# Performance work log

Measured on AMD Instinct MI355X. Metric: run time of the kernel, lower is better.

The kernel has to match this reference:

```python
import jax, jax.numpy as jnp
import numpy as np

D_MODEL = 1024
D_HIDDEN = 4096
NUM_EXPERT = 2
TOP_K = 1
W_SCALE = 0.02  # keep expert pre-exp outputs small so exp() in combine stays finite
EPS = float(np.finfo(float).eps)


def setup_inputs() -> dict:
    key = jax.random.key(0)
    ks = jax.random.split(key, 6)
    x = jax.random.normal(ks[0], (4, 4096, D_MODEL), dtype=jnp.float32)
    Wg = jax.random.normal(ks[1], (D_MODEL, NUM_EXPERT), dtype=jnp.float32) * W_SCALE
    bg = jax.random.normal(ks[2], (NUM_EXPERT,), dtype=jnp.float32) * W_SCALE
    We = jax.random.normal(ks[3], (NUM_EXPERT, D_MODEL, D_HIDDEN), dtype=jnp.float32) * W_SCALE
    be = jax.random.normal(ks[4], (NUM_EXPERT, D_HIDDEN), dtype=jnp.float32) * W_SCALE
    return {"x": x, "Wg": Wg, "bg": bg, "We": We, "be": be}


def reference(x, Wg, bg, We, be):
    B, N, C = x.shape
    xt = x.reshape(-1, C)                               # [T, C]
    # NaiveGate: linear -> top-k -> softmax over top-k logits -> dense scatter
    logits = xt @ Wg + bg                               # [T, E]
    top_v, top_i = jax.lax.top_k(logits, TOP_K)         # [T, k]
    top_g = jax.nn.softmax(top_v, axis=-1)              # [T, k] (==1.0 when k=1)
    gates = jnp.sum(jax.nn.one_hot(top_i, NUM_EXPERT, dtype=logits.dtype) * top_g[..., None], axis=1)  # [T, E]
    # expert FFNs (dense over all tokens; gate==0 tokens contribute nothing in combine,
    # matching SparseDispatcher semantics exactly)
    eo = jnp.einsum('tc,ech->eth', xt, We) + be[:, None, :]   # [E, T, H]
    # combine: sum_e gate[t,e] * exp(expert_e(x_t)); zeros -> eps; then log
    combined = jnp.einsum('te,eth->th', gates, jnp.exp(eo))   # [T, H]
    combined = jnp.where(combined == 0, EPS, combined)
    return jnp.log(combined).reshape(B, N, D_HIDDEN)
```

## Files before the change

kernel.cpp:

```cpp
#include <hip/hip_runtime.h>
#include <hip/hip_bf16.h>


#define DM 1024
#define DH 4096
#define KS 32
#define NS (DM / KS)

typedef __attribute__((ext_vector_type(4))) float f32x4;
typedef __attribute__((ext_vector_type(8))) __bf16 bf16x8;

__device__ __forceinline__ unsigned short f2bf(float f) {
    union { float f; unsigned u; } a; a.f = f;
    unsigned u = a.u;
    u += 0x7fffu + ((u >> 16) & 1u);
    return (unsigned short)(u >> 16);
}

__device__ __forceinline__ void gl16(const unsigned short* g, unsigned short* l) {
    __builtin_amdgcn_global_load_lds(
        (const __attribute__((address_space(1))) unsigned int*)(g),
        (__attribute__((address_space(3))) unsigned int*)(l), 16, 0, 0);
}

__global__ __launch_bounds__(1024) void prep(
    const float* __restrict__ x, const float* __restrict__ Wg,
    const float* __restrict__ bg, const float* __restrict__ We, int T,
    unsigned short* __restrict__ xbf, unsigned short* __restrict__ webt,
    int* __restrict__ perm, int* __restrict__ eidx, int* __restrict__ cur)
{
    int bid = blockIdx.x, tid = threadIdx.x;

    if (bid < 512) {
        __shared__ unsigned short tile[4][64][72];
        int sub = tid >> 8, t2 = tid & 255;
        int g = bid * 4 + sub;
        int e = g >> 10, rr = g & 1023, kt = rr >> 6, ht = rr & 63;
        int k0 = kt * 64, h0 = ht * 64;
        int k = t2 >> 2, hc = t2 & 3;
        const float* src = We + ((size_t)e * DM + k0 + k) * DH + h0 + hc * 16;
#pragma unroll
        for (int j = 0; j < 4; ++j) {
            f32x4 v = *(const f32x4*)(src + j * 4);
#pragma unroll
            for (int q = 0; q < 4; ++q)
                tile[sub][hc * 16 + j * 4 + q][k] = f2bf(v[q]);
        }
        __syncthreads();
        int h = t2 >> 2, kc = t2 & 3;
        unsigned short* dst = webt + ((size_t)e * DH + h0 + h) * DM + k0 + kc * 16;
        *(uint4*)(dst)     = *(const uint4*)&tile[sub][h][kc * 16];
        *(uint4*)(dst + 8) = *(const uint4*)&tile[sub][h][kc * 16 + 8];
        return;
    }

    __shared__ unsigned char eL[64];
    int gb = bid - 512;
    int lane = tid & 63, w = tid >> 6;
    float wgv[32];
#pragma unroll
    for (int j = 0; j < 8; ++j)
        *(f32x4*)&wgv[j * 4] = *(const f32x4*)(Wg + lane * 32 + j * 4);
    float bg0 = bg[0], bg1 = bg[1];
    int t0 = gb * 64 + w * 4;
#pragma unroll
    for (int tl = 0; tl < 4; ++tl) {
        int t = t0 + tl;
        const float* xr = x + (size_t)t * DM + lane * 16;
        double g0 = 0.0, g1 = 0.0;
        unsigned hw[8];
#pragma unroll
        for (int j = 0; j < 4; ++j) {
            f32x4 v = *(const f32x4*)(xr + j * 4);
#pragma unroll
            for (int q = 0; q < 4; ++q) {
                g0 += (double)v[q] * (double)wgv[2 * (j * 4 + q)];
                g1 += (double)v[q] * (double)wgv[2 * (j * 4 + q) + 1];
            }
            hw[j * 2]     = (unsigned)f2bf(v[0]) | ((unsigned)f2bf(v[1]) << 16);
            hw[j * 2 + 1] = (unsigned)f2bf(v[2]) | ((unsigned)f2bf(v[3]) << 16);
        }
        unsigned short* xw = xbf + (size_t)t * DM + lane * 16;
        uint4 u0; u0.x = hw[0]; u0.y = hw[1]; u0.z = hw[2]; u0.w = hw[3];
        uint4 u1; u1.x = hw[4]; u1.y = hw[5]; u1.z = hw[6]; u1.w = hw[7];
        *(uint4*)(xw)     = u0;
        *(uint4*)(xw + 8) = u1;
#pragma unroll
        for (int off = 32; off; off >>= 1) {
            g0 += __shfl_xor(g0, off);
            g1 += __shfl_xor(g1, off);
        }
        if (lane == 0) {
            int ee = ((g1 + (double)bg1) > (g0 + (double)bg0)) ? 1 : 0;
            eidx[t] = ee;
            eL[w * 4 + tl] = (unsigned char)ee;
        }
    }
    __syncthreads();
    if (w == 0) {
        int myE = eL[lane];
        unsigned long long m1 = __ballot(myE != 0);
        int tot1 = __popcll(m1);
        int b0 = 0, b1 = 0;
        if (lane == 0) {
            b0 = atomicAdd(cur, 64 - tot1);
            b1 = atomicAdd(cur + 1, tot1);
        }
        b0 = __shfl(b0, 0);
        b1 = __shfl(b1, 0);
        unsigned long long lm = (1ull << lane) - 1ull;
        int rank = __popcll((myE ? m1 : ~m1) & lm);
        int dstp = myE ? (T - b1 - tot1 + rank) : (b0 + rank);
        perm[dstp] = gb * 64 + lane;
    }
}

__global__ __launch_bounds__(256, 3) void moe_gemm(
    const unsigned short* __restrict__ xbf,
    const unsigned short* __restrict__ webt,
    const float* __restrict__ be,
    const int* __restrict__ perm,
    const int* __restrict__ eidx,
    float* __restrict__ out)
{
    __shared__ __align__(16) char smem[17408];
    unsigned short* As = (unsigned short*)smem;
    unsigned short* Bs = (unsigned short*)(smem + 8192);

    const int nwg = gridDim.x;
    const int bid = blockIdx.x;
    const int swz = (bid & 7) * (nwg >> 3) + (bid >> 3);
    const int mt = swz >> 5, nt = swz & 31;
    const int m0 = mt * 128, n0 = nt * 128;
    const int tid = threadIdx.x, lane = tid & 63, wid = tid >> 6;
    const int wm = wid >> 1, wn = wid & 1;

    const unsigned short *aptr0, *aptr1;
    size_t bofs0, bofs1;
    {
        int c0 = tid, c1 = tid + 256;
        int r0 = c0 >> 2, k80 = (c0 & 3) ^ ((r0 >> 1) & 3);
        int r1 = c1 >> 2, k81 = (c1 & 3) ^ ((r1 >> 1) & 3);
        aptr0 = xbf + (size_t)perm[m0 + r0] * DM + k80 * 8;
        aptr1 = xbf + (size_t)perm[m0 + r1] * DM + k81 * 8;
        bofs0 = (size_t)(n0 + r0) * DM + k80 * 8;
        bofs1 = (size_t)(n0 + r1) * DM + k81 * 8;
    }

    const int rA = wm * 64 + (lane & 15);
    const int rB = wn * 64 + (lane & 15);
    const int offA = rA * KS + (((lane >> 4) ^ ((rA >> 1) & 3)) * 8);
    const int offB = rB * KS + (((lane >> 4) ^ ((rB >> 1) & 3)) * 8);

    const int e_lo = eidx[perm[m0]];
    const int e_hi = eidx[perm[m0 + 127]];

    for (int e = e_lo; e <= e_hi; ++e) {
        const unsigned short* wb = webt + (size_t)e * DH * DM;

        f32x4 acc[4][4];
#pragma unroll
        for (int mi = 0; mi < 4; ++mi)
#pragma unroll
            for (int ni = 0; ni < 4; ++ni) acc[mi][ni] = 0.f;

#pragma unroll 1
        for (int kt = 0; kt < NS; ++kt) {
            __syncthreads();
            gl16(aptr0 + kt * KS, As + tid * 8);
            gl16(aptr1 + kt * KS, As + (tid + 256) * 8);
            gl16(wb + bofs0 + kt * KS, Bs + tid * 8);
            gl16(wb + bofs1 + kt * KS, Bs + (tid + 256) * 8);
            __syncthreads();

            bf16x8 af[4], bfr[4];
#pragma unroll
            for (int mi = 0; mi < 4; ++mi) af[mi] = *(const bf16x8*)(As + offA + mi * 16 * KS);
#pragma unroll
            for (int ni = 0; ni < 4; ++ni) bfr[ni] = *(const bf16x8*)(Bs + offB + ni * 16 * KS);
#pragma unroll
            for (int mi = 0; mi < 4; ++mi)
#pragma unroll
                for (int ni = 0; ni < 4; ++ni)
                    acc[mi][ni] = __builtin_amdgcn_mfma_f32_16x16x32_bf16(
                        af[mi], bfr[ni], acc[mi][ni], 0, 0, 0);
        }

        __syncthreads();
        float* ep = (float*)smem + wid * (16 * 68);
        const int colb = n0 + wn * 64;
        float bev[4];
#pragma unroll
        for (int ni = 0; ni < 4; ++ni) bev[ni] = be[e * DH + colb + ni * 16 + (lane & 15)];
        const bool multi = (e_lo != e_hi);
        const int rowb = m0 + wm * 64;

#pragma unroll
        for (int mi = 0; mi < 4; ++mi) {
#pragma unroll
            for (int ni = 0; ni < 4; ++ni)
#pragma unroll
                for (int r = 0; r < 4; ++r)
                    ep[((lane >> 4) * 4 + r) * 68 + ni * 16 + (lane & 15)] =
                        acc[mi][ni][r] + bev[ni];
#pragma unroll
            for (int g = 0; g < 4; ++g) {
                f32x4 v = *(const f32x4*)&ep[(g * 4 + (lane >> 4)) * 68 + (lane & 15) * 4];
                int tk = perm[rowb + mi * 16 + g * 4 + (lane >> 4)];
                if (!multi || eidx[tk] == e)
                    __builtin_nontemporal_store(
                        v, (f32x4*)(out + (size_t)tk * DH + colb + (lane & 15) * 4));
            }
        }
    }
}

extern "C" void kernel_launch(void* const* d_in, const int* in_sizes, int n_in,
                              void* d_out, int out_size, void* d_ws, size_t ws_size,
                              hipStream_t stream) {
    const float* x  = (const float*)d_in[0];
    const float* Wg = (const float*)d_in[1];
    const float* bg = (const float*)d_in[2];
    const float* We = (const float*)d_in[3];
    const float* be = (const float*)d_in[4];
    float* out = (float*)d_out;
    int T = in_sizes[0] / DM;

    char* ws = (char*)d_ws;
    int* cur  = (int*)ws;
    int* perm = (int*)(ws + 4096);
    int* eidx = (int*)(ws + 4096 + 65536);
    unsigned short* webt = (unsigned short*)(ws + 4096 + 2 * 65536);
    unsigned short* xbf  = (unsigned short*)(ws + 4096 + 2 * 65536 + (size_t)2 * DH * DM * 2);

    hipMemsetAsync(cur, 0, 8, stream);
    hipLaunchKernelGGL(prep, dim3(512 + T / 64), dim3(1024), 0, stream,
                       x, Wg, bg, We, T, xbf, webt, perm, eidx, cur);
    int nblk = (T / 128) * (DH / 128);
    hipLaunchKernelGGL(moe_gemm, dim3(nblk), dim3(256), 0, stream,
                       xbf, webt, be, perm, eidx, out);
}
```

Baseline: 223.7 us.

## Triple-buffer LDS tiles with two-stage async prefetch in MoE GEMM

Replaces the single-buffered load/sync/compute K loop with a three-slot LDS ring: two stages are prefetched via global_load_lds before the loop, and each iteration issues the load for kt+2 before computing kt. Explicit vmcnt waits and one barrier per iteration replace the two __syncthreads. The aim is to hide global memory latency behind MFMA work. LDS use grows from 17 KB to 48 KB per block, which may lower occupancy below the launch-bounds target of 3 blocks.

```diff
diff --git a/kernel.cpp b/kernel.cpp
--- a/kernel.cpp
+++ b/kernel.cpp
@@ -123,9 +123,7 @@
     const int* __restrict__ eidx,
     float* __restrict__ out)
 {
-    __shared__ __align__(16) char smem[17408];
-    unsigned short* As = (unsigned short*)smem;
-    unsigned short* Bs = (unsigned short*)(smem + 8192);
+    __shared__ __align__(16) char smem[3 * 16384];
 
     const int nwg = gridDim.x;
     const int bid = blockIdx.x;
@@ -158,21 +156,42 @@
     for (int e = e_lo; e <= e_hi; ++e) {
         const unsigned short* wb = webt + (size_t)e * DH * DM;
 
+        __syncthreads();
+
+#pragma unroll
+        for (int s = 0; s < 2; ++s) {
+            unsigned short* Asl = (unsigned short*)(smem + s * 16384);
+            unsigned short* Bsl = (unsigned short*)(smem + s * 16384 + 8192);
+            gl16(aptr0 + s * KS, Asl + tid * 8);
+            gl16(aptr1 + s * KS, Asl + (tid + 256) * 8);
+            gl16(wb + bofs0 + s * KS, Bsl + tid * 8);
+            gl16(wb + bofs1 + s * KS, Bsl + (tid + 256) * 8);
+        }
+
         f32x4 acc[4][4];
 #pragma unroll
         for (int mi = 0; mi < 4; ++mi)
 #pragma unroll
             for (int ni = 0; ni < 4; ++ni) acc[mi][ni] = 0.f;
 
+        asm volatile("s_waitcnt vmcnt(4)" ::: "memory");
+        __builtin_amdgcn_s_barrier();
+
+        unsigned o_cur = 0, o_nxt = 16384, o_pf = 32768;
 #pragma unroll 1
         for (int kt = 0; kt < NS; ++kt) {
-            __syncthreads();
-            gl16(aptr0 + kt * KS, As + tid * 8);
-            gl16(aptr1 + kt * KS, As + (tid + 256) * 8);
-            gl16(wb + bofs0 + kt * KS, Bs + tid * 8);
-            gl16(wb + bofs1 + kt * KS, Bs + (tid + 256) * 8);
-            __syncthreads();
-
+            if (kt + 2 < NS) {
+                unsigned short* Asl = (unsigned short*)(smem + o_pf);
+                unsigned short* Bsl = (unsigned short*)(smem + o_pf + 8192);
+                gl16(aptr0 + (kt + 2) * KS, Asl + tid * 8);
+                gl16(aptr1 + (kt + 2) * KS, Asl + (tid + 256) * 8);
+                gl16(wb + bofs0 + (kt + 2) * KS, Bsl + tid * 8);
+                gl16(wb + bofs1 + (kt + 2) * KS, Bsl + (tid + 256) * 8);
+            }
+            __builtin_amdgcn_sched_barrier(0);
+
+            const unsigned short* As = (const unsigned short*)(smem + o_cur);
+            const unsigned short* Bs = (const unsigned short*)(smem + o_cur + 8192);
             bf16x8 af[4], bfr[4];
 #pragma unroll
             for (int mi = 0; mi < 4; ++mi) af[mi] = *(const bf16x8*)(As + offA + mi * 16 * KS);
@@ -184,9 +203,16 @@
                 for (int ni = 0; ni < 4; ++ni)
                     acc[mi][ni] = __builtin_amdgcn_mfma_f32_16x16x32_bf16(
                         af[mi], bfr[ni], acc[mi][ni], 0, 0, 0);
-        }
-
-        __syncthreads();
+
+            __builtin_amdgcn_sched_barrier(0);
+            if (kt < NS - 2) asm volatile("s_waitcnt vmcnt(4)" ::: "memory");
+            else             asm volatile("s_waitcnt vmcnt(0)" ::: "memory");
+            __builtin_amdgcn_s_barrier();
+            __builtin_amdgcn_sched_barrier(0);
+
+            unsigned t = o_cur; o_cur = o_nxt; o_nxt = o_pf; o_pf = t;
+        }
+
         float* ep = (float*)smem + wid * (16 * 68);
         const int colb = n0 + wn * 64;
         float bev[4];
```

Result: slower. 232.7 us (+4.0%).

## Triple-buffer LDS loads with register prefetch and remap tiles per XCD

Applied to the files above, without the earlier changes.

Replaces the single-buffered K loop (two barriers per step) with a three-stage LDS ring fed by async global-to-LDS loads. Each step waits on vmcnt and issues a single barrier, prefetches fragments into registers one stage ahead, and raises wave priority around the MFMA block. The block-to-tile mapping is also changed so each XCD works on a contiguous band of M tiles, which should improve L2 reuse of activations and weights. LDS use grows to 48KB per block, which may lower occupancy below the launch bound of 3 blocks per CU, and the hand-written waitcnt and barrier sequencing is fragile.

```diff
diff --git a/kernel.cpp b/kernel.cpp
--- a/kernel.cpp
+++ b/kernel.cpp
@@ -123,17 +123,23 @@
     const int* __restrict__ eidx,
     float* __restrict__ out)
 {
-    __shared__ __align__(16) char smem[17408];
-    unsigned short* As = (unsigned short*)smem;
-    unsigned short* Bs = (unsigned short*)(smem + 8192);
-
-    const int nwg = gridDim.x;
+    __shared__ __align__(16) char smem[3 * 16384];
+
     const int bid = blockIdx.x;
-    const int swz = (bid & 7) * (nwg >> 3) + (bid >> 3);
-    const int mt = swz >> 5, nt = swz & 31;
+    const int xcd = bid & 7, idx = bid >> 3;
+    const int st = idx >> 5, q = idx & 31;
+    const int mt = xcd * 16 + (st >> 3) * 8 + (q >> 2);
+    const int nt = (st & 7) * 4 + (q & 3);
     const int m0 = mt * 128, n0 = nt * 128;
     const int tid = threadIdx.x, lane = tid & 63, wid = tid >> 6;
     const int wm = wid >> 1, wn = wid & 1;
+
+    unsigned short* const A0 = (unsigned short*)(smem);
+    unsigned short* const B0 = (unsigned short*)(smem + 8192);
+    unsigned short* const A1 = (unsigned short*)(smem + 16384);
+    unsigned short* const B1 = (unsigned short*)(smem + 24576);
+    unsigned short* const A2 = (unsigned short*)(smem + 32768);
+    unsigned short* const B2 = (unsigned short*)(smem + 40960);
 
     const unsigned short *aptr0, *aptr1;
     size_t bofs0, bofs1;
@@ -158,33 +164,92 @@
     for (int e = e_lo; e <= e_hi; ++e) {
         const unsigned short* wb = webt + (size_t)e * DH * DM;
 
+        __syncthreads();
+
+        gl16(aptr0,            A0 + tid * 8);
+        gl16(aptr1,            A0 + (tid + 256) * 8);
+        gl16(webt + (size_t)e * DH * DM + bofs0, B0 + tid * 8);
+        gl16(webt + (size_t)e * DH * DM + bofs1, B0 + (tid + 256) * 8);
+        gl16(aptr0 + KS,       A1 + tid * 8);
+        gl16(aptr1 + KS,       A1 + (tid + 256) * 8);
+        gl16(wb + bofs0 + KS,  B1 + tid * 8);
+        gl16(wb + bofs1 + KS,  B1 + (tid + 256) * 8);
+        gl16(aptr0 + 2 * KS,   A2 + tid * 8);
+        gl16(aptr1 + 2 * KS,   A2 + (tid + 256) * 8);
+        gl16(wb + bofs0 + 2 * KS, B2 + tid * 8);
+        gl16(wb + bofs1 + 2 * KS, B2 + (tid + 256) * 8);
+
         f32x4 acc[4][4];
 #pragma unroll
         for (int mi = 0; mi < 4; ++mi)
 #pragma unroll
             for (int ni = 0; ni < 4; ++ni) acc[mi][ni] = 0.f;
 
+        asm volatile("s_waitcnt vmcnt(4)" ::: "memory");
+        __builtin_amdgcn_s_barrier();
+        __builtin_amdgcn_sched_barrier(0);
+
+        const unsigned short* ga0 = aptr0 + 3 * KS;
+        const unsigned short* ga1 = aptr1 + 3 * KS;
+        const unsigned short* gb0 = wb + bofs0 + 3 * KS;
+        const unsigned short* gb1 = wb + bofs1 + 3 * KS;
+
+        bf16x8 fa0[4], fb0[4], fa1[4], fb1[4];
+#pragma unroll
+        for (int mi = 0; mi < 4; ++mi) fa0[mi] = *(const bf16x8*)(A0 + offA + mi * 16 * KS);
+#pragma unroll
+        for (int ni = 0; ni < 4; ++ni) fb0[ni] = *(const bf16x8*)(B0 + offB + ni * 16 * KS);
+
+#define STAGE(AS, BS) { \
+        gl16(ga0, AS + tid * 8); gl16(ga1, AS + (tid + 256) * 8); \
+        gl16(gb0, BS + tid * 8); gl16(gb1, BS + (tid + 256) * 8); \
+        ga0 += KS; ga1 += KS; gb0 += KS; gb1 += KS; }
+
+#define LOADF(AS, BS, FA, FB) { \
+        _Pragma("unroll") \
+        for (int mi = 0; mi < 4; ++mi) FA[mi] = *(const bf16x8*)(AS + offA + mi * 16 * KS); \
+        _Pragma("unroll") \
+        for (int ni = 0; ni < 4; ++ni) FB[ni] = *(const bf16x8*)(BS + offB + ni * 16 * KS); }
+
+#define MM(FA, FB) { \
+        __builtin_amdgcn_s_setprio(1); \
+        _Pragma("unroll") \
+        for (int mi = 0; mi < 4; ++mi) \
+        _Pragma("unroll") \
+            for (int ni = 0; ni < 4; ++ni) \
+                acc[mi][ni] = __builtin_amdgcn_mfma_f32_16x16x32_bf16(FA[mi], FB[ni], acc[mi][ni], 0, 0, 0); \
+        __builtin_amdgcn_s_setprio(0); }
+
+#define WAIT4 { __builtin_amdgcn_sched_barrier(0); \
+        asm volatile("s_waitcnt vmcnt(4)" ::: "memory"); \
+        __builtin_amdgcn_s_barrier(); __builtin_amdgcn_sched_barrier(0); }
+
 #pragma unroll 1
-        for (int kt = 0; kt < NS; ++kt) {
-            __syncthreads();
-            gl16(aptr0 + kt * KS, As + tid * 8);
-            gl16(aptr1 + kt * KS, As + (tid + 256) * 8);
-            gl16(wb + bofs0 + kt * KS, Bs + tid * 8);
-            gl16(wb + bofs1 + kt * KS, Bs + (tid + 256) * 8);
-            __syncthreads();
-
-            bf16x8 af[4], bfr[4];
-#pragma unroll
-            for (int mi = 0; mi < 4; ++mi) af[mi] = *(const bf16x8*)(As + offA + mi * 16 * KS);
-#pragma unroll
-            for (int ni = 0; ni < 4; ++ni) bfr[ni] = *(const bf16x8*)(Bs + offB + ni * 16 * KS);
-#pragma unroll
-            for (int mi = 0; mi < 4; ++mi)
-#pragma unroll
-                for (int ni = 0; ni < 4; ++ni)
-                    acc[mi][ni] = __builtin_amdgcn_mfma_f32_16x16x32_bf16(
-                        af[mi], bfr[ni], acc[mi][ni], 0, 0, 0);
-        }
+        for (int u = 0; u < 4; ++u) {
+            STAGE(A0, B0); LOADF(A1, B1, fa1, fb1); MM(fa0, fb0); WAIT4;
+            STAGE(A1, B1); LOADF(A2, B2, fa0, fb0); MM(fa1, fb1); WAIT4;
+            STAGE(A2, B2); LOADF(A0, B0, fa1, fb1); MM(fa0, fb0); WAIT4;
+            STAGE(A0, B0); LOADF(A1, B1, fa0, fb0); MM(fa1, fb1); WAIT4;
+            STAGE(A1, B1); LOADF(A2, B2, fa1, fb1); MM(fa0, fb0); WAIT4;
+            STAGE(A2, B2); LOADF(A0, B0, fa0, fb0); MM(fa1, fb1); WAIT4;
+        }
+        STAGE(A0, B0); LOADF(A1, B1, fa1, fb1); MM(fa0, fb0); WAIT4;
+        STAGE(A1, B1); LOADF(A2, B2, fa0, fb0); MM(fa1, fb1); WAIT4;
+        STAGE(A2, B2); LOADF(A0, B0, fa1, fb1); MM(fa0, fb0); WAIT4;
+        STAGE(A0, B0); LOADF(A1, B1, fa0, fb0); MM(fa1, fb1); WAIT4;
+        STAGE(A1, B1); LOADF(A2, B2, fa1, fb1); MM(fa0, fb0); WAIT4;
+        LOADF(A0, B0, fa0, fb0); MM(fa1, fb1);
+        __builtin_amdgcn_sched_barrier(0);
+        asm volatile("s_waitcnt vmcnt(0)" ::: "memory");
+        __builtin_amdgcn_s_barrier();
+        __builtin_amdgcn_sched_barrier(0);
+        LOADF(A1, B1, fa1, fb1); MM(fa0, fb0);
+        MM(fa1, fb1);
+
+#undef STAGE
+#undef LOADF
+#undef MM
+#undef WAIT4
 
         __syncthreads();
         float* ep = (float*)smem + wid * (16 * 68);
```

Result: no change. 224.3 us (+0.3%).

## Load MFMA fragments directly from global with register double-buffering

Applied to the files above, without the earlier changes.

Drops the LDS staging of A and B tiles. Each wave now loads its bf16 MFMA fragments straight from global memory into registers, double-buffered across k-steps, with s_setprio raised around the MFMA blocks. This removes two barriers per k-step and the LDS round trip. In exchange, each wave fetches its fragments separately, so the shared A/B rows are read several times from L2 instead of once per block. The tile-to-block mapping is also changed to group tiles per XCD in 8x4 supertiles for L2 locality, and a barrier is added after the epilogue.

```diff
diff --git a/kernel.cpp b/kernel.cpp
--- a/kernel.cpp
+++ b/kernel.cpp
@@ -15,12 +15,6 @@
     unsigned u = a.u;
     u += 0x7fffu + ((u >> 16) & 1u);
     return (unsigned short)(u >> 16);
-}
-
-__device__ __forceinline__ void gl16(const unsigned short* g, unsigned short* l) {
-    __builtin_amdgcn_global_load_lds(
-        (const __attribute__((address_space(1))) unsigned int*)(g),
-        (__attribute__((address_space(3))) unsigned int*)(l), 16, 0, 0);
 }
 
 __global__ __launch_bounds__(1024) void prep(
@@ -123,40 +117,35 @@
     const int* __restrict__ eidx,
     float* __restrict__ out)
 {
-    __shared__ __align__(16) char smem[17408];
-    unsigned short* As = (unsigned short*)smem;
-    unsigned short* Bs = (unsigned short*)(smem + 8192);
-
-    const int nwg = gridDim.x;
+    __shared__ __align__(16) float ep_s[4 * 16 * 68];
+
     const int bid = blockIdx.x;
-    const int swz = (bid & 7) * (nwg >> 3) + (bid >> 3);
-    const int mt = swz >> 5, nt = swz & 31;
+    const int xcd = bid & 7, idx = bid >> 3;
+    const int st = idx >> 5, q = idx & 31;
+    const int mt = xcd * 16 + (st >> 3) * 8 + (q >> 2);
+    const int nt = (st & 7) * 4 + (q & 3);
     const int m0 = mt * 128, n0 = nt * 128;
     const int tid = threadIdx.x, lane = tid & 63, wid = tid >> 6;
     const int wm = wid >> 1, wn = wid & 1;
 
-    const unsigned short *aptr0, *aptr1;
-    size_t bofs0, bofs1;
-    {
-        int c0 = tid, c1 = tid + 256;
-        int r0 = c0 >> 2, k80 = (c0 & 3) ^ ((r0 >> 1) & 3);
-        int r1 = c1 >> 2, k81 = (c1 & 3) ^ ((r1 >> 1) & 3);
-        aptr0 = xbf + (size_t)perm[m0 + r0] * DM + k80 * 8;
-        aptr1 = xbf + (size_t)perm[m0 + r1] * DM + k81 * 8;
-        bofs0 = (size_t)(n0 + r0) * DM + k80 * 8;
-        bofs1 = (size_t)(n0 + r1) * DM + k81 * 8;
-    }
-
-    const int rA = wm * 64 + (lane & 15);
-    const int rB = wn * 64 + (lane & 15);
-    const int offA = rA * KS + (((lane >> 4) ^ ((rA >> 1) & 3)) * 8);
-    const int offB = rB * KS + (((lane >> 4) ^ ((rB >> 1) & 3)) * 8);
+    const int lr = lane & 15, lg = lane >> 4;
+    const unsigned short* pa[4];
+#pragma unroll
+    for (int mi = 0; mi < 4; ++mi) {
+        int row = wm * 64 + lr + mi * 16;
+        pa[mi] = xbf + (size_t)perm[m0 + row] * DM + lg * 8;
+    }
 
     const int e_lo = eidx[perm[m0]];
     const int e_hi = eidx[perm[m0 + 127]];
 
     for (int e = e_lo; e <= e_hi; ++e) {
-        const unsigned short* wb = webt + (size_t)e * DH * DM;
+        const unsigned short* pb[4];
+#pragma unroll
+        for (int ni = 0; ni < 4; ++ni) {
+            int row = n0 + wn * 64 + lr + ni * 16;
+            pb[ni] = webt + (size_t)e * DH * DM + (size_t)row * DM + lg * 8;
+        }
 
         f32x4 acc[4][4];
 #pragma unroll
@@ -164,34 +153,39 @@
 #pragma unroll
             for (int ni = 0; ni < 4; ++ni) acc[mi][ni] = 0.f;
 
+#define LOADG(FA, FB, KT) { \
+        _Pragma("unroll") \
+        for (int mi = 0; mi < 4; ++mi) FA[mi] = *(const bf16x8*)(pa[mi] + (KT) * KS); \
+        _Pragma("unroll") \
+        for (int ni = 0; ni < 4; ++ni) FB[ni] = *(const bf16x8*)(pb[ni] + (KT) * KS); }
+
+#define MM(FA, FB) { \
+        __builtin_amdgcn_s_setprio(1); \
+        _Pragma("unroll") \
+        for (int mi = 0; mi < 4; ++mi) \
+        _Pragma("unroll") \
+            for (int ni = 0; ni < 4; ++ni) \
+                acc[mi][ni] = __builtin_amdgcn_mfma_f32_16x16x32_bf16(FA[mi], FB[ni], acc[mi][ni], 0, 0, 0); \
+        __builtin_amdgcn_s_setprio(0); }
+
+        bf16x8 fa0[4], fb0[4], fa1[4], fb1[4];
+        LOADG(fa0, fb0, 0);
 #pragma unroll 1
-        for (int kt = 0; kt < NS; ++kt) {
-            __syncthreads();
-            gl16(aptr0 + kt * KS, As + tid * 8);
-            gl16(aptr1 + kt * KS, As + (tid + 256) * 8);
-            gl16(wb + bofs0 + kt * KS, Bs + tid * 8);
-            gl16(wb + bofs1 + kt * KS, Bs + (tid + 256) * 8);
-            __syncthreads();
-
-            bf16x8 af[4], bfr[4];
-#pragma unroll
-            for (int mi = 0; mi < 4; ++mi) af[mi] = *(const bf16x8*)(As + offA + mi * 16 * KS);
-#pragma unroll
-            for (int ni = 0; ni < 4; ++ni) bfr[ni] = *(const bf16x8*)(Bs + offB + ni * 16 * KS);
-#pragma unroll
-            for (int mi = 0; mi < 4; ++mi)
-#pragma unroll
-                for (int ni = 0; ni < 4; ++ni)
-                    acc[mi][ni] = __builtin_amdgcn_mfma_f32_16x16x32_bf16(
-                        af[mi], bfr[ni], acc[mi][ni], 0, 0, 0);
-        }
+        for (int kt = 0; kt < NS; kt += 2) {
+            LOADG(fa1, fb1, kt + 1);
+            MM(fa0, fb0);
+            if (kt + 2 < NS) LOADG(fa0, fb0, kt + 2);
+            MM(fa1, fb1);
+        }
+#undef LOADG
+#undef MM
 
         __syncthreads();
-        float* ep = (float*)smem + wid * (16 * 68);
+        float* ep = ep_s + wid * (16 * 68);
         const int colb = n0 + wn * 64;
         float bev[4];
 #pragma unroll
-        for (int ni = 0; ni < 4; ++ni) bev[ni] = be[e * DH + colb + ni * 16 + (lane & 15)];
+        for (int ni = 0; ni < 4; ++ni) bev[ni] = be[e * DH + colb + ni * 16 + lr];
         const bool multi = (e_lo != e_hi);
         const int rowb = m0 + wm * 64;
 
@@ -201,17 +195,17 @@
             for (int ni = 0; ni < 4; ++ni)
 #pragma unroll
                 for (int r = 0; r < 4; ++r)
-                    ep[((lane >> 4) * 4 + r) * 68 + ni * 16 + (lane & 15)] =
-                        acc[mi][ni][r] + bev[ni];
+                    ep[(lg * 4 + r) * 68 + ni * 16 + lr] = acc[mi][ni][r] + bev[ni];
 #pragma unroll
             for (int g = 0; g < 4; ++g) {
-                f32x4 v = *(const f32x4*)&ep[(g * 4 + (lane >> 4)) * 68 + (lane & 15) * 4];
-                int tk = perm[rowb + mi * 16 + g * 4 + (lane >> 4)];
+                f32x4 v = *(const f32x4*)&ep[(g * 4 + lg) * 68 + lr * 4];
+                int tk = perm[rowb + mi * 16 + g * 4 + lg];
                 if (!multi || eidx[tk] == e)
                     __builtin_nontemporal_store(
-                        v, (f32x4*)(out + (size_t)tk * DH + colb + (lane & 15) * 4));
+                        v, (f32x4*)(out + (size_t)tk * DH + colb + lr * 4));
             }
         }
+        __syncthreads();
     }
 }
 
```

After: 562.0 us. 151% more time.
